# Performance work log

Measured on AMD Instinct MI355X. Metric: run time of the kernel, lower is better.

Reference implementation:

```python
import jax, jax.numpy as jnp
import numpy as np

TOKEN_DIM = 256
TPR_DIM = 12
INNER_DIM = 256
HID = 32
BN_EPS = 1e-5
SCALE = TOKEN_DIM ** (-0.5)


def setup_inputs() -> dict:
    key = jax.random.key(0)
    ks = jax.random.split(key, 12)
    B, T = 2, 512
    x = jax.random.normal(ks[0], (B, T, TOKEN_DIM), dtype=jnp.float32)
    r = jax.random.normal(ks[1], (B, T, T, TPR_DIM), dtype=jnp.float32)
    # tpr_mlp params
    w1 = jax.random.normal(ks[2], (TPR_DIM, HID), dtype=jnp.float32) * (TPR_DIM ** -0.5)
    b1 = jnp.zeros((HID,), jnp.float32)
    g1 = jnp.ones((HID,), jnp.float32) + 0.1 * jax.random.normal(ks[3], (HID,), dtype=jnp.float32)
    be1 = 0.1 * jax.random.normal(ks[4], (HID,), dtype=jnp.float32)
    m1 = 0.1 * jax.random.normal(ks[5], (HID,), dtype=jnp.float32)
    v1 = jnp.ones((HID,), jnp.float32) + 0.1 * jax.random.uniform(ks[6], (HID,), dtype=jnp.float32)
    w2 = jax.random.normal(ks[7], (HID, TOKEN_DIM), dtype=jnp.float32) * (HID ** -0.5)
    b2 = jnp.zeros((TOKEN_DIM,), jnp.float32)
    g2 = jnp.ones((TOKEN_DIM,), jnp.float32) + 0.1 * jax.random.normal(ks[8], (TOKEN_DIM,), dtype=jnp.float32)
    be2 = 0.1 * jax.random.normal(ks[9], (TOKEN_DIM,), dtype=jnp.float32)
    m2 = 0.1 * jax.random.normal(ks[10], (TOKEN_DIM,), dtype=jnp.float32)
    v2 = jnp.ones((TOKEN_DIM,), jnp.float32) + 0.1 * jax.random.uniform(ks[11], (TOKEN_DIM,), dtype=jnp.float32)
    w_qkv = jax.random.normal(jax.random.fold_in(key, 99), (TOKEN_DIM, 3 * INNER_DIM), dtype=jnp.float32) * (TOKEN_DIM ** -0.5)
    return {"x": x, "r": r, "w1": w1, "b1": b1, "g1": g1, "be1": be1, "m1": m1, "v1": v1,
            "w2": w2, "b2": b2, "g2": g2, "be2": be2, "m2": m2, "v2": v2, "w_qkv": w_qkv}


def _bn_relu(h, g, be, m, v):
    # BatchNorm1d (eval mode, running stats) followed by ReLU; broadcasts over leading dims
    return jax.nn.relu((h - m) * jax.lax.rsqrt(v + BN_EPS) * g + be)


def reference(x, r, w1, b1, g1, be1, m1, v1, w2, b2, g2, be2, m2, v2, w_qkv):
    # TPR MLP over [B,T,T,tpr_dim]
    h = _bn_relu(jnp.einsum('bstd,dh->bsth', r, w1) + b1, g1, be1, m1, v1)   # [B,T,T,HID]
    h = _bn_relu(jnp.einsum('bsth,hc->bstc', h, w2) + b2, g2, be2, m2, v2)    # [B,T,T,C]
    bias = jnp.max(h, axis=2)                                                 # [B,T,C]
    xb = x + bias
    qkv = jnp.einsum('btc,ce->bte', xb, w_qkv)                                # [B,T,3*INNER]
    q, k, v_ = jnp.split(qkv, 3, axis=-1)
    dots = jnp.einsum('btd,bsd->bts', q, k) * SCALE                           # [B,T,T]
    attn = jax.nn.softmax(dots, axis=-1)
    out = jnp.einsum('bts,bsd->btd', attn, v_)                                # [B,T,INNER]
    return out
```

## Files before the change

### kernel.cpp

```cpp
#include <hip/hip_runtime.h>
#include <hip/hip_bf16.h>

#define T 512
#define C 256
#define D12 12
#define HID 32
#define BN_EPS 1e-5f
#define SCALE 0.0625f

typedef __attribute__((ext_vector_type(8))) short bf16x8;
typedef __attribute__((ext_vector_type(4))) float f32x4;

static __device__ __forceinline__ short f2bf(float f) {
    __hip_bfloat16 h = __float2bfloat16(f);
    return *reinterpret_cast<short*>(&h);
}

__global__ __launch_bounds__(256) void k1_mlp_bias(
    const float* __restrict__ x, const float* __restrict__ r,
    const float* __restrict__ w1, const float* __restrict__ b1,
    const float* __restrict__ g1, const float* __restrict__ be1,
    const float* __restrict__ m1, const float* __restrict__ v1,
    const float* __restrict__ w2, const float* __restrict__ b2,
    const float* __restrict__ g2, const float* __restrict__ be2,
    const float* __restrict__ m2, const float* __restrict__ v2,
    short* __restrict__ xbb)
{
    __shared__ float s1sh[HID];
    __shared__ float C1sh[HID];
    __shared__ short w1t[32 * 32];
    __shared__ short rshbf[64 * 40];
    __shared__ short h1sh[64 * 40];
    __shared__ float biassh[C];

    const int tid  = threadIdx.x;
    const int lane = tid & 63;
    const int wave = tid >> 6;
    const int quad = lane >> 4;
    const int mrow = lane & 15;
    const int blk  = blockIdx.x;

    if (tid < HID) {
        float s1 = g1[tid] * rsqrtf(v1[tid] + BN_EPS);
        s1sh[tid] = s1;
        C1sh[tid] = (b1[tid] - m1[tid]) * s1 + be1[tid];
    }
    __syncthreads();

    #pragma unroll
    for (int i = 0; i < 4; ++i) {
        int idx = i * 256 + tid;
        int h = idx >> 5, d = idx & 31;
        float v = (d < D12) ? w1[d * HID + h] * s1sh[h] : 0.f;
        w1t[h * 32 + d] = f2bf(v);
    }
    #pragma unroll
    for (int i = 0; i < 7; ++i) {
        int idx = i * 256 + tid;
        int row = idx / 28, d = 12 + idx % 28;
        rshbf[row * 40 + d] = 0;
    }

    bf16x8 bfrag[4];
    float  c2r[4];
    #pragma unroll
    for (int ct = 0; ct < 4; ++ct) {
        int c = wave * 64 + ct * 16 + mrow;
        float s2 = g2[c] * rsqrtf(v2[c] + BN_EPS);
        c2r[ct] = (b2[c] - m2[c]) * s2 + be2[c];
        #pragma unroll
        for (int j = 0; j < 8; ++j) {
            int k = quad * 8 + j;
            bfrag[ct][j] = f2bf(w2[k * C + c] * s2);
        }
    }
    __syncthreads();

    bf16x8 b1f[2];
    float  c1r[2];
    #pragma unroll
    for (int nt = 0; nt < 2; ++nt) {
        b1f[nt] = *reinterpret_cast<const bf16x8*>(&w1t[(nt * 16 + mrow) * 32 + quad * 8]);
        c1r[nt] = C1sh[nt * 16 + mrow];
    }

    const float* rbase = r + (size_t)blk * T * D12;
    float maxv[4] = {0.f, 0.f, 0.f, 0.f};

    for (int t0 = 0; t0 < T; t0 += 64) {
        #pragma unroll
        for (int i = 0; i < 3; ++i) {
            int idx = i * 256 + tid;
            int row = idx / 12, d = idx - row * 12;
            rshbf[row * 40 + d] = f2bf(rbase[t0 * D12 + idx]);
        }
        __syncthreads();
        {
            bf16x8 af = *reinterpret_cast<const bf16x8*>(
                &rshbf[(wave * 16 + mrow) * 40 + quad * 8]);
            #pragma unroll
            for (int nt = 0; nt < 2; ++nt) {
                f32x4 a = {c1r[nt], c1r[nt], c1r[nt], c1r[nt]};
                a = __builtin_amdgcn_mfma_f32_16x16x32_bf16(af, b1f[nt], a, 0, 0, 0);
                #pragma unroll
                for (int rg = 0; rg < 4; ++rg)
                    h1sh[(wave * 16 + quad * 4 + rg) * 40 + nt * 16 + mrow] =
                        f2bf(fmaxf(a[rg], 0.f));
            }
        }
        __syncthreads();
        #pragma unroll
        for (int rt = 0; rt < 4; ++rt) {
            bf16x8 a2 = *reinterpret_cast<const bf16x8*>(
                &h1sh[(rt * 16 + mrow) * 40 + quad * 8]);
            #pragma unroll
            for (int ct = 0; ct < 4; ++ct) {
                f32x4 acc = {c2r[ct], c2r[ct], c2r[ct], c2r[ct]};
                acc = __builtin_amdgcn_mfma_f32_16x16x32_bf16(a2, bfrag[ct], acc, 0, 0, 0);
                #pragma unroll
                for (int rg = 0; rg < 4; ++rg)
                    maxv[ct] = fmaxf(maxv[ct], acc[rg]);
            }
        }
        __syncthreads();
    }

    #pragma unroll
    for (int ct = 0; ct < 4; ++ct) {
        float m = maxv[ct];
        m = fmaxf(m, __shfl_xor(m, 16));
        m = fmaxf(m, __shfl_xor(m, 32));
        if (quad == 0) biassh[wave * 64 + ct * 16 + mrow] = m;
    }
    __syncthreads();
    xbb[(size_t)blk * C + tid] = f2bf(x[(size_t)blk * C + tid] + biassh[tid]);
}

__global__ __launch_bounds__(256) void k0_transpose(
    const float* __restrict__ w, short* __restrict__ wT)
{
    __shared__ short tsh[64 * 66];
    const int tid = threadIdx.x;
    const int d0 = (blockIdx.x / 12) * 64;
    const int e0 = (blockIdx.x % 12) * 64;
    #pragma unroll
    for (int i = 0; i < 16; ++i) {
        int idx = i * 256 + tid;
        int di = idx >> 6, ej = idx & 63;
        tsh[di * 66 + ej] = f2bf(w[(size_t)(d0 + di) * 768 + e0 + ej]);
    }
    __syncthreads();
    #pragma unroll
    for (int i = 0; i < 16; ++i) {
        int idx = i * 256 + tid;
        int ei = idx >> 6, dj = idx & 63;
        wT[(size_t)(e0 + ei) * 256 + d0 + dj] = tsh[dj * 66 + ei];
    }
}

__global__ __launch_bounds__(256) void k2_qkv(
    const short* __restrict__ xbb,
    const short* __restrict__ wT,
    short* __restrict__ qbf)
{
    const int tid  = threadIdx.x;
    const int lane = tid & 63;
    const int wave = tid >> 6;
    const int quad = lane >> 4;
    const int mrow = lane & 15;
    const int rb = blockIdx.x / 12;
    const int cb = blockIdx.x % 12;
    const int row0 = rb * 64 + wave * 16;
    const int col0 = cb * 64;
    const float osc = (cb < 4) ? SCALE : 1.0f;

    f32x4 acc[4];
    #pragma unroll
    for (int ct = 0; ct < 4; ++ct) acc[ct] = (f32x4){0.f, 0.f, 0.f, 0.f};

    for (int ks = 0; ks < 8; ++ks) {
        bf16x8 afrag = *reinterpret_cast<const bf16x8*>(
            &xbb[(size_t)(row0 + mrow) * 256 + ks * 32 + quad * 8]);
        #pragma unroll
        for (int ct = 0; ct < 4; ++ct) {
            bf16x8 bfrag = *reinterpret_cast<const bf16x8*>(
                &wT[(size_t)(col0 + ct * 16 + mrow) * 256 + ks * 32 + quad * 8]);
            acc[ct] = __builtin_amdgcn_mfma_f32_16x16x32_bf16(afrag, bfrag, acc[ct], 0, 0, 0);
        }
    }
    #pragma unroll
    for (int ct = 0; ct < 4; ++ct)
        #pragma unroll
        for (int rg = 0; rg < 4; ++rg)
            qbf[(size_t)(row0 + quad * 4 + rg) * 768 + col0 + ct * 16 + mrow] =
                f2bf(acc[ct][rg] * osc);
}

__global__ __launch_bounds__(256) void k2b_vtrans(
    const short* __restrict__ qbf, short* __restrict__ vT)
{
    __shared__ short tsh[64 * 66];
    const int tid = threadIdx.x;
    const int r0 = (blockIdx.x >> 2) * 64;
    const int c0 = (blockIdx.x & 3) * 64;
    #pragma unroll
    for (int i = 0; i < 16; ++i) {
        int idx = i * 256 + tid;
        int ri = idx >> 6, cj = idx & 63;
        tsh[ri * 66 + cj] = qbf[(size_t)(r0 + ri) * 768 + 512 + c0 + cj];
    }
    __syncthreads();
    const int b  = r0 >> 9;
    const int rb = r0 & 511;
    #pragma unroll
    for (int i = 0; i < 16; ++i) {
        int idx = i * 256 + tid;
        int ci = idx >> 6, rj = idx & 63;
        vT[((size_t)(b * 256 + c0 + ci)) * 512 + rb + rj] = tsh[rj * 66 + ci];
    }
}

__global__ __launch_bounds__(256) void k3a_attn(
    const short* __restrict__ qbf,
    const short* __restrict__ vT,
    float* __restrict__ po,
    float2* __restrict__ stats)
{
    __shared__ float msh[4][16];
    __shared__ float lsh[4][16];
    __shared__ short psh[16 * 136];
    const int tid  = threadIdx.x;
    const int lane = tid & 63;
    const int wave = tid >> 6;
    const int quad = lane >> 4;
    const int mrow = lane & 15;
    const int qt = blockIdx.x >> 2;
    const int sc = blockIdx.x & 3;
    const int b  = qt >> 5;
    const int row0  = qt * 16;
    const int srow0 = b * 512 + sc * 128;

    bf16x8 qf[8];
    {
        const short* qrow = qbf + (size_t)(row0 + mrow) * 768;
        #pragma unroll
        for (int ks = 0; ks < 8; ++ks)
            qf[ks] = *reinterpret_cast<const bf16x8*>(qrow + ks * 32 + quad * 8);
    }

    f32x4 S[2];
    #pragma unroll
    for (int st = 0; st < 2; ++st) {
        f32x4 acc = {0.f, 0.f, 0.f, 0.f};
        const short* krow = qbf + (size_t)(srow0 + wave * 32 + st * 16 + mrow) * 768 + 256;
        #pragma unroll
        for (int ks = 0; ks < 8; ++ks) {
            bf16x8 kf = *reinterpret_cast<const bf16x8*>(krow + ks * 32 + quad * 8);
            acc = __builtin_amdgcn_mfma_f32_16x16x32_bf16(qf[ks], kf, acc, 0, 0, 0);
        }
        S[st] = acc;
    }

    float mx[4];
    #pragma unroll
    for (int rg = 0; rg < 4; ++rg) mx[rg] = fmaxf(S[0][rg], S[1][rg]);
    #pragma unroll
    for (int off = 1; off < 16; off <<= 1)
        #pragma unroll
        for (int rg = 0; rg < 4; ++rg) mx[rg] = fmaxf(mx[rg], __shfl_xor(mx[rg], off));
    if (mrow == 0)
        #pragma unroll
        for (int rg = 0; rg < 4; ++rg) msh[wave][quad * 4 + rg] = mx[rg];
    __syncthreads();

    float M[4], sm[4];
    #pragma unroll
    for (int rg = 0; rg < 4; ++rg) {
        int m = quad * 4 + rg;
        M[rg] = fmaxf(fmaxf(msh[0][m], msh[1][m]), fmaxf(msh[2][m], msh[3][m]));
    }
    float ex[2][4];
    #pragma unroll
    for (int st = 0; st < 2; ++st)
        #pragma unroll
        for (int rg = 0; rg < 4; ++rg) ex[st][rg] = __expf(S[st][rg] - M[rg]);
    #pragma unroll
    for (int rg = 0; rg < 4; ++rg) sm[rg] = ex[0][rg] + ex[1][rg];
    #pragma unroll
    for (int off = 1; off < 16; off <<= 1)
        #pragma unroll
        for (int rg = 0; rg < 4; ++rg) sm[rg] += __shfl_xor(sm[rg], off);
    if (mrow == 0)
        #pragma unroll
        for (int rg = 0; rg < 4; ++rg) lsh[wave][quad * 4 + rg] = sm[rg];
    #pragma unroll
    for (int st = 0; st < 2; ++st)
        #pragma unroll
        for (int rg = 0; rg < 4; ++rg)
            psh[(quad * 4 + rg) * 136 + wave * 32 + st * 16 + mrow] = f2bf(ex[st][rg]);
    __syncthreads();

    if (wave == 0 && mrow == 0) {
        #pragma unroll
        for (int rg = 0; rg < 4; ++rg) {
            int m = quad * 4 + rg;
            float l = lsh[0][m] + lsh[1][m] + lsh[2][m] + lsh[3][m];
            stats[blockIdx.x * 16 + m] = make_float2(M[rg], l);
        }
    }

    const short* vbase = vT + (size_t)b * 256 * 512;
    f32x4 o[4];
    #pragma unroll
    for (int i = 0; i < 4; ++i) o[i] = (f32x4){0.f, 0.f, 0.f, 0.f};
    #pragma unroll
    for (int ks = 0; ks < 4; ++ks) {
        bf16x8 pf = *reinterpret_cast<const bf16x8*>(&psh[mrow * 136 + ks * 32 + quad * 8]);
        #pragma unroll
        for (int i = 0; i < 4; ++i) {
            int d0 = (wave * 4 + i) * 16;
            bf16x8 vf = *reinterpret_cast<const bf16x8*>(
                vbase + (size_t)(d0 + mrow) * 512 + sc * 128 + ks * 32 + quad * 8);
            o[i] = __builtin_amdgcn_mfma_f32_16x16x32_bf16(pf, vf, o[i], 0, 0, 0);
        }
    }
    #pragma unroll
    for (int i = 0; i < 4; ++i)
        #pragma unroll
        for (int rg = 0; rg < 4; ++rg)
            po[((size_t)blockIdx.x * 16 + quad * 4 + rg) * 256 + (wave * 4 + i) * 16 + mrow] =
                o[i][rg];
}

__global__ __launch_bounds__(256) void k3b_combine(
    const float* __restrict__ po, const float2* __restrict__ stats,
    float* __restrict__ out)
{
    const int row = blockIdx.x;
    const int qt = row >> 4, m = row & 15;
    const int c = threadIdx.x;
    float2 s0 = stats[(qt * 4 + 0) * 16 + m];
    float2 s1 = stats[(qt * 4 + 1) * 16 + m];
    float2 s2 = stats[(qt * 4 + 2) * 16 + m];
    float2 s3 = stats[(qt * 4 + 3) * 16 + m];
    float M = fmaxf(fmaxf(s0.x, s1.x), fmaxf(s2.x, s3.x));
    float a0 = __expf(s0.x - M), a1 = __expf(s1.x - M);
    float a2 = __expf(s2.x - M), a3 = __expf(s3.x - M);
    float inv = 1.f / (a0 * s0.y + a1 * s1.y + a2 * s2.y + a3 * s3.y);
    float acc = a0 * po[((size_t)(qt * 4 + 0) * 16 + m) * 256 + c]
              + a1 * po[((size_t)(qt * 4 + 1) * 16 + m) * 256 + c]
              + a2 * po[((size_t)(qt * 4 + 2) * 16 + m) * 256 + c]
              + a3 * po[((size_t)(qt * 4 + 3) * 16 + m) * 256 + c];
    out[(size_t)row * 256 + c] = acc * inv;
}

extern "C" void kernel_launch(void* const* d_in, const int* in_sizes, int n_in,
                              void* d_out, int out_size, void* d_ws, size_t ws_size,
                              hipStream_t stream) {
    const float* x    = (const float*)d_in[0];
    const float* r    = (const float*)d_in[1];
    const float* w1   = (const float*)d_in[2];
    const float* b1   = (const float*)d_in[3];
    const float* g1   = (const float*)d_in[4];
    const float* be1  = (const float*)d_in[5];
    const float* m1   = (const float*)d_in[6];
    const float* v1   = (const float*)d_in[7];
    const float* w2   = (const float*)d_in[8];
    const float* b2   = (const float*)d_in[9];
    const float* g2   = (const float*)d_in[10];
    const float* be2  = (const float*)d_in[11];
    const float* m2   = (const float*)d_in[12];
    const float* v2   = (const float*)d_in[13];
    const float* wqkv = (const float*)d_in[14];
    float* out = (float*)d_out;

    char* ws = (char*)d_ws;
    short*  qbf   = (short*)(ws);
    short*  vT    = (short*)(ws + 1572864);
    short*  xbb   = (short*)(ws + 2097152);
    short*  wT    = (short*)(ws + 2621440);
    float*  po    = (float*)(ws + 3014656);
    float2* stats = (float2*)(ws + 7208960);

    k0_transpose<<<48, 256, 0, stream>>>(wqkv, wT);
    k1_mlp_bias<<<1024, 256, 0, stream>>>(x, r, w1, b1, g1, be1, m1, v1,
                                          w2, b2, g2, be2, m2, v2, xbb);
    k2_qkv<<<192, 256, 0, stream>>>(xbb, wT, qbf);
    k2b_vtrans<<<64, 256, 0, stream>>>(qbf, vT);
    k3a_attn<<<256, 256, 0, stream>>>(qbf, vT, po, stats);
    k3b_combine<<<1024, 256, 0, stream>>>(po, stats, out);
}
```

Measured before the change: 136.6 us.

## Split TPR MLP into separate layer-1 kernel and barrier-free layer-2 max kernel

The fused MLP+max kernel is split in two. A new kernel computes layer 1 with scalar FMAs, reading r as float4 and writing h1 in bf16 to workspace. The second kernel streams h1 straight from global memory into MFMA with no shared memory or barriers. It also hoists the per-channel bias add and ReLU of layer 2 out of the max loop, relying on max and monotone ReLU commuting. In exchange it adds a 32 MB bf16 h1 round trip through global memory and one extra launch.

```diff
diff --git a/kernel.cpp b/kernel.cpp
--- a/kernel.cpp
+++ b/kernel.cpp
@@ -16,23 +16,65 @@
     return *reinterpret_cast<short*>(&h);
 }
 
-__global__ __launch_bounds__(256) void k1_mlp_bias(
-    const float* __restrict__ x, const float* __restrict__ r,
+__global__ __launch_bounds__(256) void k1a_h1(
+    const float* __restrict__ r,
     const float* __restrict__ w1, const float* __restrict__ b1,
     const float* __restrict__ g1, const float* __restrict__ be1,
     const float* __restrict__ m1, const float* __restrict__ v1,
+    short* __restrict__ h1bf)
+{
+    __shared__ float w1sh[D12 * HID];
+    __shared__ float C1sh[HID];
+    const int tid = threadIdx.x;
+    if (tid < HID) {
+        float s1 = g1[tid] * rsqrtf(v1[tid] + BN_EPS);
+        C1sh[tid] = (b1[tid] - m1[tid]) * s1 + be1[tid];
+        for (int d = 0; d < D12; ++d)
+            w1sh[d * HID + tid] = w1[d * HID + tid] * s1;
+    }
+    __syncthreads();
+
+    const int row0 = blockIdx.x * 1024 + tid;
+    float rv[4][12];
+    #pragma unroll
+    for (int j = 0; j < 4; ++j) {
+        const float4* p = reinterpret_cast<const float4*>(r + (size_t)(row0 + 256 * j) * D12);
+        float4 a = p[0], b = p[1], c = p[2];
+        rv[j][0] = a.x; rv[j][1] = a.y; rv[j][2]  = a.z; rv[j][3]  = a.w;
+        rv[j][4] = b.x; rv[j][5] = b.y; rv[j][6]  = b.z; rv[j][7]  = b.w;
+        rv[j][8] = c.x; rv[j][9] = c.y; rv[j][10] = c.z; rv[j][11] = c.w;
+    }
+
+    for (int hb = 0; hb < 4; ++hb) {
+        bf16x8 o[4];
+        #pragma unroll
+        for (int hh = 0; hh < 8; ++hh) {
+            int h = hb * 8 + hh;
+            float c0 = C1sh[h];
+            float acc[4] = {c0, c0, c0, c0};
+            #pragma unroll
+            for (int d = 0; d < D12; ++d) {
+                float w = w1sh[d * HID + h];
+                #pragma unroll
+                for (int j = 0; j < 4; ++j) acc[j] += rv[j][d] * w;
+            }
+            #pragma unroll
+            for (int j = 0; j < 4; ++j) o[j][hh] = f2bf(fmaxf(acc[j], 0.f));
+        }
+        #pragma unroll
+        for (int j = 0; j < 4; ++j)
+            *reinterpret_cast<bf16x8*>(h1bf + (size_t)(row0 + 256 * j) * HID + hb * 8) = o[j];
+    }
+}
+
+__global__ __launch_bounds__(256) void k1b_l2max(
+    const short* __restrict__ h1bf, const float* __restrict__ x,
     const float* __restrict__ w2, const float* __restrict__ b2,
     const float* __restrict__ g2, const float* __restrict__ be2,
     const float* __restrict__ m2, const float* __restrict__ v2,
     short* __restrict__ xbb)
 {
-    __shared__ float s1sh[HID];
-    __shared__ float C1sh[HID];
-    __shared__ short w1t[32 * 32];
-    __shared__ short rshbf[64 * 40];
-    __shared__ short h1sh[64 * 40];
     __shared__ float biassh[C];
-
     const int tid  = threadIdx.x;
     const int lane = tid & 63;
     const int wave = tid >> 6;
@@ -40,27 +82,6 @@
     const int mrow = lane & 15;
     const int blk  = blockIdx.x;
 
-    if (tid < HID) {
-        float s1 = g1[tid] * rsqrtf(v1[tid] + BN_EPS);
-        s1sh[tid] = s1;
-        C1sh[tid] = (b1[tid] - m1[tid]) * s1 + be1[tid];
-    }
-    __syncthreads();
-
-    #pragma unroll
-    for (int i = 0; i < 4; ++i) {
-        int idx = i * 256 + tid;
-        int h = idx >> 5, d = idx & 31;
-        float v = (d < D12) ? w1[d * HID + h] * s1sh[h] : 0.f;
-        w1t[h * 32 + d] = f2bf(v);
-    }
-    #pragma unroll
-    for (int i = 0; i < 7; ++i) {
-        int idx = i * 256 + tid;
-        int row = idx / 28, d = 12 + idx % 28;
-        rshbf[row * 40 + d] = 0;
-    }
-
     bf16x8 bfrag[4];
     float  c2r[4];
     #pragma unroll
@@ -69,68 +90,29 @@
         float s2 = g2[c] * rsqrtf(v2[c] + BN_EPS);
         c2r[ct] = (b2[c] - m2[c]) * s2 + be2[c];
         #pragma unroll
-        for (int j = 0; j < 8; ++j) {
-            int k = quad * 8 + j;
-            bfrag[ct][j] = f2bf(w2[k * C + c] * s2);
-        }
-    }
-    __syncthreads();
-
-    bf16x8 b1f[2];
-    float  c1r[2];
-    #pragma unroll
-    for (int nt = 0; nt < 2; ++nt) {
-        b1f[nt] = *reinterpret_cast<const bf16x8*>(&w1t[(nt * 16 + mrow) * 32 + quad * 8]);
-        c1r[nt] = C1sh[nt * 16 + mrow];
-    }
-
-    const float* rbase = r + (size_t)blk * T * D12;
-    float maxv[4] = {0.f, 0.f, 0.f, 0.f};
-
-    for (int t0 = 0; t0 < T; t0 += 64) {
-        #pragma unroll
-        for (int i = 0; i < 3; ++i) {
-            int idx = i * 256 + tid;
-            int row = idx / 12, d = idx - row * 12;
-            rshbf[row * 40 + d] = f2bf(rbase[t0 * D12 + idx]);
-        }
-        __syncthreads();
-        {
-            bf16x8 af = *reinterpret_cast<const bf16x8*>(
-                &rshbf[(wave * 16 + mrow) * 40 + quad * 8]);
-            #pragma unroll
-            for (int nt = 0; nt < 2; ++nt) {
-                f32x4 a = {c1r[nt], c1r[nt], c1r[nt], c1r[nt]};
-                a = __builtin_amdgcn_mfma_f32_16x16x32_bf16(af, b1f[nt], a, 0, 0, 0);
-                #pragma unroll
-                for (int rg = 0; rg < 4; ++rg)
-                    h1sh[(wave * 16 + quad * 4 + rg) * 40 + nt * 16 + mrow] =
-                        f2bf(fmaxf(a[rg], 0.f));
-            }
-        }
-        __syncthreads();
-        #pragma unroll
-        for (int rt = 0; rt < 4; ++rt) {
-            bf16x8 a2 = *reinterpret_cast<const bf16x8*>(
-                &h1sh[(rt * 16 + mrow) * 40 + quad * 8]);
-            #pragma unroll
-            for (int ct = 0; ct < 4; ++ct) {
-                f32x4 acc = {c2r[ct], c2r[ct], c2r[ct], c2r[ct]};
-                acc = __builtin_amdgcn_mfma_f32_16x16x32_bf16(a2, bfrag[ct], acc, 0, 0, 0);
-                #pragma unroll
-                for (int rg = 0; rg < 4; ++rg)
-                    maxv[ct] = fmaxf(maxv[ct], acc[rg]);
-            }
-        }
-        __syncthreads();
-    }
-
+        for (int j = 0; j < 8; ++j)
+            bfrag[ct][j] = f2bf(w2[(quad * 8 + j) * C + c] * s2);
+    }
+
+    const short* hbase = h1bf + (size_t)blk * T * HID;
+    float maxv[4] = {-1e30f, -1e30f, -1e30f, -1e30f};
+    #pragma unroll 4
+    for (int rt = 0; rt < 32; ++rt) {
+        bf16x8 af = *reinterpret_cast<const bf16x8*>(
+            hbase + (size_t)(rt * 16 + mrow) * HID + quad * 8);
+        #pragma unroll
+        for (int ct = 0; ct < 4; ++ct) {
+            f32x4 acc = {0.f, 0.f, 0.f, 0.f};
+            acc = __builtin_amdgcn_mfma_f32_16x16x32_bf16(af, bfrag[ct], acc, 0, 0, 0);
+            maxv[ct] = fmaxf(maxv[ct], fmaxf(fmaxf(acc[0], acc[1]), fmaxf(acc[2], acc[3])));
+        }
+    }
     #pragma unroll
     for (int ct = 0; ct < 4; ++ct) {
         float m = maxv[ct];
         m = fmaxf(m, __shfl_xor(m, 16));
         m = fmaxf(m, __shfl_xor(m, 32));
-        if (quad == 0) biassh[wave * 64 + ct * 16 + mrow] = m;
+        if (quad == 0) biassh[wave * 64 + ct * 16 + mrow] = fmaxf(m + c2r[ct], 0.f);
     }
     __syncthreads();
     xbb[(size_t)blk * C + tid] = f2bf(x[(size_t)blk * C + tid] + biassh[tid]);
@@ -159,8 +141,7 @@
 }
 
 __global__ __launch_bounds__(256) void k2_qkv(
-    const short* __restrict__ xbb,
-    const short* __restrict__ wT,
+    const short* __restrict__ xbb, const short* __restrict__ wT,
     short* __restrict__ qbf)
 {
     const int tid  = threadIdx.x;
@@ -221,10 +202,8 @@
 }
 
 __global__ __launch_bounds__(256) void k3a_attn(
-    const short* __restrict__ qbf,
-    const short* __restrict__ vT,
-    float* __restrict__ po,
-    float2* __restrict__ stats)
+    const short* __restrict__ qbf, const short* __restrict__ vT,
+    float* __restrict__ po, float2* __restrict__ stats)
 {
     __shared__ float msh[4][16];
     __shared__ float lsh[4][16];
@@ -381,10 +360,11 @@
     short*  wT    = (short*)(ws + 2621440);
     float*  po    = (float*)(ws + 3014656);
     float2* stats = (float2*)(ws + 7208960);
+    short*  h1bf  = (short*)(ws + 8388608);
 
     k0_transpose<<<48, 256, 0, stream>>>(wqkv, wT);
-    k1_mlp_bias<<<1024, 256, 0, stream>>>(x, r, w1, b1, g1, be1, m1, v1,
-                                          w2, b2, g2, be2, m2, v2, xbb);
+    k1a_h1<<<512, 256, 0, stream>>>(r, w1, b1, g1, be1, m1, v1, h1bf);
+    k1b_l2max<<<1024, 256, 0, stream>>>(h1bf, x, w2, b2, g2, be2, m2, v2, xbb);
     k2_qkv<<<192, 256, 0, stream>>>(xbb, wT, qbf);
     k2b_vtrans<<<64, 256, 0, stream>>>(qbf, vT);
     k3a_attn<<<256, 256, 0, stream>>>(qbf, vT, po, stats);
```

Measured after the change: 157.7 us. 15.5% more time.

## Make MLP-bias kernel wave-independent and defer second BN-ReLU past the max

Applied to the files above, without the earlier changes.

Each wave in the MLP kernel now handles its own 128 rows of r across all 256 output channels. It uses private shared-memory tiles, so the per-tile __syncthreads barriers are gone and only a final cross-wave max reduction remains. The second-layer bias and ReLU are applied once after the max over t instead of per element. This relies on max commuting with a monotone affine map, which needs the BN scale to be positive. Each wave now holds 16 B fragments and 16 running maxima in registers, which raises register pressure and may lower occupancy.

```diff
diff --git a/kernel.cpp b/kernel.cpp
--- a/kernel.cpp
+++ b/kernel.cpp
@@ -16,7 +16,7 @@
     return *reinterpret_cast<short*>(&h);
 }
 
-__global__ __launch_bounds__(256) void k1_mlp_bias(
+__global__ __launch_bounds__(256) void k1w_mlp_bias(
     const float* __restrict__ x, const float* __restrict__ r,
     const float* __restrict__ w1, const float* __restrict__ b1,
     const float* __restrict__ g1, const float* __restrict__ be1,
@@ -26,13 +26,9 @@
     const float* __restrict__ m2, const float* __restrict__ v2,
     short* __restrict__ xbb)
 {
-    __shared__ float s1sh[HID];
-    __shared__ float C1sh[HID];
-    __shared__ short w1t[32 * 32];
-    __shared__ short rshbf[64 * 40];
-    __shared__ short h1sh[64 * 40];
-    __shared__ float biassh[C];
-
+    __shared__ short rp[4][16 * 40];
+    __shared__ short h1p[4][16 * 40];
+    __shared__ float bsh[4][C];
     const int tid  = threadIdx.x;
     const int lane = tid & 63;
     const int wave = tid >> 6;
@@ -40,100 +36,90 @@
     const int mrow = lane & 15;
     const int blk  = blockIdx.x;
 
-    if (tid < HID) {
-        float s1 = g1[tid] * rsqrtf(v1[tid] + BN_EPS);
-        s1sh[tid] = s1;
-        C1sh[tid] = (b1[tid] - m1[tid]) * s1 + be1[tid];
-    }
-    __syncthreads();
-
-    #pragma unroll
-    for (int i = 0; i < 4; ++i) {
-        int idx = i * 256 + tid;
-        int h = idx >> 5, d = idx & 31;
-        float v = (d < D12) ? w1[d * HID + h] * s1sh[h] : 0.f;
-        w1t[h * 32 + d] = f2bf(v);
-    }
+    short* rw = &rp[wave][0];
+    short* hw = &h1p[wave][0];
+
     #pragma unroll
     for (int i = 0; i < 7; ++i) {
-        int idx = i * 256 + tid;
+        int idx = i * 64 + lane;
         int row = idx / 28, d = 12 + idx % 28;
-        rshbf[row * 40 + d] = 0;
-    }
-
-    bf16x8 bfrag[4];
-    float  c2r[4];
-    #pragma unroll
-    for (int ct = 0; ct < 4; ++ct) {
-        int c = wave * 64 + ct * 16 + mrow;
-        float s2 = g2[c] * rsqrtf(v2[c] + BN_EPS);
-        c2r[ct] = (b2[c] - m2[c]) * s2 + be2[c];
+        rw[row * 40 + d] = 0;
+    }
+
+    bf16x8 b1f[2];
+    float  c1i[2];
+    #pragma unroll
+    for (int nt = 0; nt < 2; ++nt) {
+        int h = nt * 16 + mrow;
+        float s1 = g1[h] * rsqrtf(v1[h] + BN_EPS);
+        c1i[nt] = (b1[h] - m1[h]) * s1 + be1[h];
         #pragma unroll
         for (int j = 0; j < 8; ++j) {
             int k = quad * 8 + j;
-            bfrag[ct][j] = f2bf(w2[k * C + c] * s2);
-        }
-    }
-    __syncthreads();
-
-    bf16x8 b1f[2];
-    float  c1r[2];
-    #pragma unroll
-    for (int nt = 0; nt < 2; ++nt) {
-        b1f[nt] = *reinterpret_cast<const bf16x8*>(&w1t[(nt * 16 + mrow) * 32 + quad * 8]);
-        c1r[nt] = C1sh[nt * 16 + mrow];
-    }
-
-    const float* rbase = r + (size_t)blk * T * D12;
-    float maxv[4] = {0.f, 0.f, 0.f, 0.f};
-
-    for (int t0 = 0; t0 < T; t0 += 64) {
+            b1f[nt][j] = (k < D12) ? f2bf(w1[k * HID + h] * s1) : (short)0;
+        }
+    }
+
+    bf16x8 b2f[16];
+    #pragma unroll
+    for (int ct = 0; ct < 16; ++ct) {
+        int c = ct * 16 + mrow;
+        float s2 = g2[c] * rsqrtf(v2[c] + BN_EPS);
+        #pragma unroll
+        for (int j = 0; j < 8; ++j)
+            b2f[ct][j] = f2bf(w2[(quad * 8 + j) * C + c] * s2);
+    }
+
+    const float* rb = r + ((size_t)blk * T + wave * 128) * D12;
+    float maxv[16];
+    #pragma unroll
+    for (int ct = 0; ct < 16; ++ct) maxv[ct] = -1e30f;
+
+    for (int tile = 0; tile < 8; ++tile) {
         #pragma unroll
         for (int i = 0; i < 3; ++i) {
-            int idx = i * 256 + tid;
+            int idx = i * 64 + lane;
             int row = idx / 12, d = idx - row * 12;
-            rshbf[row * 40 + d] = f2bf(rbase[t0 * D12 + idx]);
-        }
-        __syncthreads();
+            rw[row * 40 + d] = f2bf(rb[tile * 192 + idx]);
+        }
         {
-            bf16x8 af = *reinterpret_cast<const bf16x8*>(
-                &rshbf[(wave * 16 + mrow) * 40 + quad * 8]);
+            bf16x8 af = *reinterpret_cast<const bf16x8*>(&rw[mrow * 40 + quad * 8]);
             #pragma unroll
             for (int nt = 0; nt < 2; ++nt) {
-                f32x4 a = {c1r[nt], c1r[nt], c1r[nt], c1r[nt]};
+                f32x4 a = {c1i[nt], c1i[nt], c1i[nt], c1i[nt]};
                 a = __builtin_amdgcn_mfma_f32_16x16x32_bf16(af, b1f[nt], a, 0, 0, 0);
                 #pragma unroll
                 for (int rg = 0; rg < 4; ++rg)
-                    h1sh[(wave * 16 + quad * 4 + rg) * 40 + nt * 16 + mrow] =
-                        f2bf(fmaxf(a[rg], 0.f));
+                    hw[(quad * 4 + rg) * 40 + nt * 16 + mrow] = f2bf(fmaxf(a[rg], 0.f));
             }
         }
-        __syncthreads();
-        #pragma unroll
-        for (int rt = 0; rt < 4; ++rt) {
-            bf16x8 a2 = *reinterpret_cast<const bf16x8*>(
-                &h1sh[(rt * 16 + mrow) * 40 + quad * 8]);
+        {
+            bf16x8 a2 = *reinterpret_cast<const bf16x8*>(&hw[mrow * 40 + quad * 8]);
             #pragma unroll
-            for (int ct = 0; ct < 4; ++ct) {
-                f32x4 acc = {c2r[ct], c2r[ct], c2r[ct], c2r[ct]};
-                acc = __builtin_amdgcn_mfma_f32_16x16x32_bf16(a2, bfrag[ct], acc, 0, 0, 0);
-                #pragma unroll
-                for (int rg = 0; rg < 4; ++rg)
-                    maxv[ct] = fmaxf(maxv[ct], acc[rg]);
+            for (int ct = 0; ct < 16; ++ct) {
+                f32x4 acc = {0.f, 0.f, 0.f, 0.f};
+                acc = __builtin_amdgcn_mfma_f32_16x16x32_bf16(a2, b2f[ct], acc, 0, 0, 0);
+                maxv[ct] = fmaxf(maxv[ct],
+                                 fmaxf(fmaxf(acc[0], acc[1]), fmaxf(acc[2], acc[3])));
             }
         }
-        __syncthreads();
-    }
-
-    #pragma unroll
-    for (int ct = 0; ct < 4; ++ct) {
+    }
+
+    #pragma unroll
+    for (int ct = 0; ct < 16; ++ct) {
         float m = maxv[ct];
         m = fmaxf(m, __shfl_xor(m, 16));
         m = fmaxf(m, __shfl_xor(m, 32));
-        if (quad == 0) biassh[wave * 64 + ct * 16 + mrow] = m;
-    }
-    __syncthreads();
-    xbb[(size_t)blk * C + tid] = f2bf(x[(size_t)blk * C + tid] + biassh[tid]);
+        if (quad == 0) bsh[wave][ct * 16 + mrow] = m;
+    }
+    __syncthreads();
+
+    float mraw = fmaxf(fmaxf(bsh[0][tid], bsh[1][tid]),
+                       fmaxf(bsh[2][tid], bsh[3][tid]));
+    float s2 = g2[tid] * rsqrtf(v2[tid] + BN_EPS);
+    float c2 = (b2[tid] - m2[tid]) * s2 + be2[tid];
+    float bias = fmaxf(mraw + c2, 0.f);
+    xbb[(size_t)blk * C + tid] = f2bf(x[(size_t)blk * C + tid] + bias);
 }
 
 __global__ __launch_bounds__(256) void k0_transpose(
@@ -159,8 +145,7 @@
 }
 
 __global__ __launch_bounds__(256) void k2_qkv(
-    const short* __restrict__ xbb,
-    const short* __restrict__ wT,
+    const short* __restrict__ xbb, const short* __restrict__ wT,
     short* __restrict__ qbf)
 {
     const int tid  = threadIdx.x;
@@ -221,10 +206,8 @@
 }
 
 __global__ __launch_bounds__(256) void k3a_attn(
-    const short* __restrict__ qbf,
-    const short* __restrict__ vT,
-    float* __restrict__ po,
-    float2* __restrict__ stats)
+    const short* __restrict__ qbf, const short* __restrict__ vT,
+    float* __restrict__ po, float2* __restrict__ stats)
 {
     __shared__ float msh[4][16];
     __shared__ float lsh[4][16];
@@ -383,8 +366,8 @@
     float2* stats = (float2*)(ws + 7208960);
 
     k0_transpose<<<48, 256, 0, stream>>>(wqkv, wT);
-    k1_mlp_bias<<<1024, 256, 0, stream>>>(x, r, w1, b1, g1, be1, m1, v1,
-                                          w2, b2, g2, be2, m2, v2, xbb);
+    k1w_mlp_bias<<<1024, 256, 0, stream>>>(x, r, w1, b1, g1, be1, m1, v1,
+                                           w2, b2, g2, be2, m2, v2, xbb);
     k2_qkv<<<192, 256, 0, stream>>>(xbb, wT, qbf);
     k2b_vtrans<<<64, 256, 0, stream>>>(qbf, vT);
     k3a_attn<<<256, 256, 0, stream>>>(qbf, vT, po, stats);
```

Result: slower. 143.4 us (+5.0%).
